# Performance work log

Hardware: AMD Instinct MI355X
Metric: run time of the kernel (lower is better)

The kernel has to match this reference:

```python
import jax, jax.numpy as jnp
import numpy as np

N = 50000      # nodes in the graph (len(vertices))
E = 800000     # edges per adjacency
D = 128        # n_feature (pretrained embedding dim)
V = 100000     # n_input (entity vocab)
OUT = 20       # n_output
L = 7          # n_hidden layers
BN_EPS = 1e-5


def setup_inputs() -> dict:
    key = jax.random.key(0)
    ks = jax.random.split(key, 12)
    s = 1.0 / np.sqrt(D)
    return {
        "vertices": jax.random.randint(ks[0], (N,), 0, V),
        "edge_index": jax.random.randint(ks[1], (L, 2, E), 0, N),
        "edge_weight": jax.random.uniform(ks[2], (L, E), jnp.float32),
        "emb_table": jax.random.normal(ks[3], (V, D), jnp.float32) * 0.02,
        "gcn_w_hidden": jax.random.normal(ks[4], (L - 1, D, D), jnp.float32) * s,
        "gcn_b_hidden": jnp.zeros((L - 1, D), jnp.float32),
        "gcn_w_out": jax.random.normal(ks[5], (D, OUT), jnp.float32) * s,
        "gcn_b_out": jnp.zeros((OUT,), jnp.float32),
        "bn_gamma_hidden": jnp.ones((L - 1, D), jnp.float32),
        "bn_beta_hidden": jnp.zeros((L - 1, D), jnp.float32),
        "bn_gamma_out": jnp.ones((OUT,), jnp.float32),
        "bn_beta_out": jnp.zeros((OUT,), jnp.float32),
        "te_wl": jax.random.normal(ks[6], (L - 1, D, D), jnp.float32) * s,
        "te_wc": jax.random.normal(ks[7], (L - 1, D, D), jnp.float32) * s,
        "te_b": jnp.zeros((L - 1, D), jnp.float32),
        "mask_w": jax.random.normal(ks[8], (V,), jnp.float32) * 0.02,
        "mask_b": jnp.zeros((OUT,), jnp.float32),
    }


def _spmm(src, dst, w, x):
    # out[i] = sum_{e: dst[e]==i} w[e] * x[src[e]]  (sparse adj @ x)
    return jax.ops.segment_sum(w[:, None] * x[src], dst, num_segments=N)


def _batchnorm(x, gamma, beta):
    # BatchNorm1d over the node (batch) axis, training-mode batch statistics
    m = x.mean(axis=0)
    v = x.var(axis=0)
    return (x - m) * jax.lax.rsqrt(v + BN_EPS) * gamma + beta


def reference(vertices, edge_index, edge_weight, emb_table,
              gcn_w_hidden, gcn_b_hidden, gcn_w_out, gcn_b_out,
              bn_gamma_hidden, bn_beta_hidden, bn_gamma_out, bn_beta_out,
              te_wl, te_wc, te_b, mask_w, mask_b):
    x = emb_table[vertices]                               # [N, D]
    for i in range(L):
        last_x = x
        if i < L - 1:
            support = x @ gcn_w_hidden[i]                 # [N, D]
            h = _spmm(edge_index[i, 0], edge_index[i, 1], edge_weight[i], support)
            h = h + gcn_b_hidden[i]
            h = _batchnorm(h, bn_gamma_hidden[i], bn_beta_hidden[i])
            h = jax.nn.relu(h)                            # dropout: eval mode (identity)
            j = (i - 1) % (L - 1)  # faithful to temporal_cells[i-1] (i=0 hits index -1)
            g = jax.nn.sigmoid(last_x @ te_wl[j] + h @ te_wc[j] + te_b[j])
            x = g * h + (1.0 - g) * last_x                # temporal gating cell
        else:
            support = x @ gcn_w_out                       # [N, OUT]
            h = _spmm(edge_index[i, 0], edge_index[i, 1], edge_weight[i], support)
            h = h + gcn_b_out
            x = _batchnorm(h, bn_gamma_out, bn_beta_out)
    x = jax.nn.relu(x)                                    # [N, OUT]
    out = jax.nn.sigmoid(mask_w[vertices] @ x + mask_b)   # MaskLinear + sigmoid -> [OUT]
    return out
```

## Files before the change

kernel.cpp:

```cpp
#include <hip/hip_runtime.h>
#include <hip/hip_fp16.h>

#define NN 50000
#define EE 800000
#define DIM 128
#define OUTC 20
#define LL 7
#define LE (LL*EE)
#define LN (LL*NN)
#define BN_EPS 1e-5f
#define LSTRIDE 136
#define NREP 64
#define NBUK 196
#define GMS  200
#define NBLK 200
#define CH   4000
#define CH4  (CH/4)
#define SCN  (LL*NBUK*NBLK)
#define FSCAP 4864
#define STATSZ (6*NREP*256 + 8*64 + 8*32)
#define STATSZ4 (STATSZ/4)

typedef __attribute__((ext_vector_type(8))) short short8;
typedef __attribute__((ext_vector_type(4))) float f32x4;

static __device__ __forceinline__ float sigm(float z){ return 1.0f/(1.0f+expf(-z)); }
static __device__ __forceinline__ unsigned short f2bf(float f){
  unsigned int u = __float_as_uint(f);
  u += 0x7FFF + ((u>>16)&1);
  return (unsigned short)(u>>16);
}
static __device__ __forceinline__ float bf2f(unsigned short s){
  return __uint_as_float(((unsigned int)s)<<16);
}

__global__ __launch_bounds__(256) void k_pre(const float* __restrict__ wh,
    const float* __restrict__ tewl, const float* __restrict__ tewc,
    const float* __restrict__ wout,
    unsigned short* __restrict__ Wt, unsigned short* __restrict__ WtO,
    const int* __restrict__ ei, int* __restrict__ Gm, float* __restrict__ stats){
  int bid = blockIdx.x;
  int t = threadIdx.x;
  if (bid < 1152){
    int gid = bid*256+t;
    int m = gid>>14; int idx = gid&16383;
    int n = idx>>7, k = idx&127;
    const float* src = (m<6)? wh + (size_t)m*16384
                     : (m<12)? tewl + (size_t)(m-6)*16384
                     : tewc + (size_t)(m-12)*16384;
    Wt[gid] = f2bf(src[k*128+n]);
  } else if (bid < 1168){
    int idx = (bid-1152)*256+t;
    int n = idx>>7, k = idx&127;
    WtO[idx] = (n<OUTC)? f2bf(wout[k*OUTC+n]) : (unsigned short)0;
  } else if (bid < 2568){
    int bb = bid-1168;
    int l = bb / NBLK, b = bb - l*NBLK;
    __shared__ int h[NBUK];
    if (t<NBUK) h[t]=0;
    const int4* dsts = (const int4*)(ei + (size_t)(2*l+1)*EE + b*CH);
    int4 dv[4];
    #pragma unroll
    for (int i=0;i<4;i++){
      int k4 = t + i*256;
      if (k4<CH4) dv[i] = dsts[k4];
    }
    __syncthreads();
    #pragma unroll
    for (int i=0;i<4;i++){
      int k4 = t + i*256;
      if (k4<CH4){
        atomicAdd(&h[dv[i].x>>8], 1);
        atomicAdd(&h[dv[i].y>>8], 1);
        atomicAdd(&h[dv[i].z>>8], 1);
        atomicAdd(&h[dv[i].w>>8], 1);
      }
    }
    __syncthreads();
    int* g = Gm + (size_t)(l*NBLK+b)*GMS;
    if (t<NBUK) g[t]=h[t];
  } else {
    int z = (bid-2568)*256+t;
    if (z < STATSZ4) ((float4*)stats)[z] = make_float4(0.f,0.f,0.f,0.f);
  }
}

__global__ __launch_bounds__(256) void k_scan1p(const int* __restrict__ Gm,
    int* __restrict__ part, int* __restrict__ bsums){
  __shared__ int s[256];
  int t = threadIdx.x;
  int base = blockIdx.x*4096 + t*16;
  int v[16]; int sum = 0;
  #pragma unroll
  for (int i=0;i<16;i++){
    int idx = base+i; int val = 0;
    if (idx < SCN){
      int l = idx/(NBUK*NBLK);
      int r = idx - l*(NBUK*NBLK);
      int buk = r/NBLK, b = r - buk*NBLK;
      val = Gm[(size_t)(l*NBLK+b)*GMS + buk];
    }
    v[i]=val; sum+=val;
  }
  s[t]=sum; __syncthreads();
  for (int off=1; off<256; off<<=1){
    int x = (t>=off)? s[t-off] : 0;
    __syncthreads(); s[t]+=x; __syncthreads();
  }
  if (t==255) bsums[blockIdx.x] = s[255];
  int run = s[t]-sum;
  #pragma unroll
  for (int i=0;i<16;i++){ if (base+i<SCN) part[base+i]=run; run += v[i]; }
}

__global__ __launch_bounds__(1024) void k_scan2(int* bsums, int nb){
  __shared__ int s[1024];
  int t=threadIdx.x;
  int v = (t<nb)? bsums[t]:0;
  s[t]=v; __syncthreads();
  for (int off=1; off<1024; off<<=1){
    int x=(t>=off)? s[t-off]:0; __syncthreads(); s[t]+=x; __syncthreads();
  }
  if (t<nb) bsums[t] = s[t]-v;
}

__global__ __launch_bounds__(256) void k_bscatter(const int* __restrict__ ei,
    const float* __restrict__ ew, const int* __restrict__ S,
    const int* __restrict__ bsums, const int* __restrict__ Gm,
    unsigned int* __restrict__ btmpP, unsigned char* __restrict__ btmpD){
  int l = blockIdx.x / NBLK, b = blockIdx.x - l*NBLK;
  int t = threadIdx.x;
  __shared__ int bstart[NBUK], cur[NBUK], runb[NBUK];
  __shared__ int ps[256];
  __shared__ unsigned int  ebP[CH];
  __shared__ unsigned short ebM[CH];
  const int4*   srcs = (const int4*)(ei + (size_t)(2*l)*EE + b*CH);
  const int4*   dsts = (const int4*)(ei + (size_t)(2*l+1)*EE + b*CH);
  const float4* wsrc = (const float4*)(ew + (size_t)l*EE + b*CH);
  int4 sv[4], dv[4]; float4 wv[4];
  #pragma unroll
  for (int i=0;i<4;i++){
    int k4 = t + i*256;
    if (k4<CH4){
      sv[i] = srcs[k4];
      dv[i] = dsts[k4];
      wv[i] = wsrc[k4];
    }
  }
  int v = (t<NBUK)? Gm[(size_t)(l*NBLK+b)*GMS + t] : 0;
  ps[t]=v; __syncthreads();
  for (int o=1;o<256;o<<=1){ int x=(t>=o)?ps[t-o]:0; __syncthreads(); ps[t]+=x; __syncthreads(); }
  if (t<NBUK){
    bstart[t]=ps[t]-v; cur[t]=ps[t]-v;
    int sidx = (l*NBUK+t)*NBLK + b;
    runb[t] = S[sidx] + bsums[sidx>>12];
  }
  __syncthreads();
  #define PUTE(SRC,DST,WF) { int buk=(DST)>>8; int pos=atomicAdd(&cur[buk],1); \
    unsigned short hw=__half_as_ushort(__float2half(WF)); \
    ebP[pos]=(unsigned)(SRC)|((unsigned)hw<<16); \
    ebM[pos]=(unsigned short)(((DST)&255)|(buk<<8)); }
  #pragma unroll
  for (int i=0;i<4;i++){
    int k4 = t + i*256;
    if (k4<CH4){
      PUTE(sv[i].x, dv[i].x, wv[i].x);
      PUTE(sv[i].y, dv[i].y, wv[i].y);
      PUTE(sv[i].z, dv[i].z, wv[i].z);
      PUTE(sv[i].w, dv[i].w, wv[i].w);
    }
  }
  #undef PUTE
  __syncthreads();
  for (int k=t;k<CH;k+=256){
    unsigned short m = ebM[k];
    int buk = m>>8;
    int gp = runb[buk] + (k - bstart[buk]);
    btmpP[gp] = ebP[k];
    btmpD[gp] = (unsigned char)(m&255);
  }
}

__global__ __launch_bounds__(256) void k_fsort(const unsigned int* __restrict__ btmpP,
    const unsigned char* __restrict__ btmpD, const int* __restrict__ S,
    const int* __restrict__ bsums,
    unsigned int* __restrict__ sedge, int* __restrict__ offs){
  int lbuk = blockIdx.x;
  int l = lbuk/NBUK, bl = lbuk - l*NBUK;
  int t = threadIdx.x;
  int i0 = lbuk*NBLK, i1 = i0+NBLK;
  int base = S[i0] + bsums[i0>>12];
  int end  = (i1==SCN)? LE : (S[i1] + bsums[i1>>12]);
  int nE = end - base;
  __shared__ int cnt[256], sc[256];
  __shared__ unsigned int stg[FSCAP];
  cnt[t]=0;
  __syncthreads();
  for (int k=t; k<nE; k+=256) atomicAdd(&cnt[btmpD[base+k]], 1);
  __syncthreads();
  int c = cnt[t];
  sc[t]=c;
  __syncthreads();
  for (int o=1;o<256;o<<=1){
    int v = (t>=o)? sc[t-o]:0;
    __syncthreads();
    sc[t]+=v;
    __syncthreads();
  }
  int excl = sc[t]-c;
  {
    int node = bl*256+t;
    if (node<NN) offs[(size_t)l*NN+node] = base + excl;
  }
  if (lbuk==0 && t==255) offs[LN]=LE;
  if (nE <= FSCAP){
    cnt[t] = excl;
    __syncthreads();
    for (int k=t; k<nE; k+=256){
      int d = btmpD[base+k];
      int r = atomicAdd(&cnt[d],1);
      stg[r] = btmpP[base+k];
    }
    __syncthreads();
    for (int k=t; k<nE; k+=256) sedge[base+k] = stg[k];
  } else {
    cnt[t] = base + excl;
    __syncthreads();
    for (int k=t; k<nE; k+=256){
      int d = btmpD[base+k];
      int r = atomicAdd(&cnt[d],1);
      sedge[r] = btmpP[base+k];
    }
  }
}

__global__ __launch_bounds__(256) void k_gemm_sup_emb(const int* __restrict__ verts,
    const float* __restrict__ emb, const unsigned short* __restrict__ Wt,
    unsigned short* __restrict__ Y, unsigned short* __restrict__ xout, int M){
  __shared__ unsigned short Xs[32*LSTRIDE];
  int tid = threadIdx.x;
  int row0 = blockIdx.x*32;
  #pragma unroll
  for (int it=0; it<2; it++){
    int idx = tid + it*256;
    int r = idx>>4, k8 = idx&15;
    short8 w = short8(0);
    if (row0+r < M){
      int v = verts[row0+r];
      const float4* p = (const float4*)emb + (size_t)v*32 + k8*2;
      float4 v0 = p[0], v1 = p[1];
      w[0]=(short)f2bf(v0.x); w[1]=(short)f2bf(v0.y); w[2]=(short)f2bf(v0.z); w[3]=(short)f2bf(v0.w);
      w[4]=(short)f2bf(v1.x); w[5]=(short)f2bf(v1.y); w[6]=(short)f2bf(v1.z); w[7]=(short)f2bf(v1.w);
      *(short8*)(xout + (size_t)(row0+r)*128 + k8*8) = w;
    }
    *(short8*)&Xs[r*LSTRIDE + k8*8] = w;
  }
  __syncthreads();
  int w = tid>>6, lane = tid&63, m = lane&15, q = lane>>4;
  int rw = (w&1)*16, cw = (w>>1)*64;
  f32x4 acc[4];
  #pragma unroll
  for (int nt=0;nt<4;nt++){ acc[nt][0]=0.f; acc[nt][1]=0.f; acc[nt][2]=0.f; acc[nt][3]=0.f; }
  #pragma unroll
  for (int kc=0; kc<4; kc++){
    short8 a = *(const short8*)&Xs[(rw+m)*LSTRIDE + kc*32 + 8*q];
    #pragma unroll
    for (int nt=0; nt<4; nt++){
      short8 b = *(const short8*)&Wt[(size_t)(cw+nt*16+m)*128 + kc*32 + 8*q];
      acc[nt] = __builtin_amdgcn_mfma_f32_16x16x32_bf16(a, b, acc[nt], 0,0,0);
    }
  }
  #pragma unroll
  for (int nt=0; nt<4; nt++){
    #pragma unroll
    for (int i=0;i<4;i++){
      int rr = row0 + rw + 4*q + i;
      if (rr<M) Y[(size_t)rr*128 + cw + nt*16 + m] = f2bf(acc[nt][i]);
    }
  }
}

template<int FUSE>
__global__ __launch_bounds__(256,4) void k_gemm_gate2(const unsigned short* __restrict__ H,
    const float* __restrict__ stL,
    const float* __restrict__ gamma, const float* __restrict__ beta,
    const unsigned short* __restrict__ Wl, const unsigned short* __restrict__ Wc,
    const unsigned short* __restrict__ Wn, const float* __restrict__ teb,
    unsigned short* __restrict__ x, unsigned short* __restrict__ supY, int M){
  __shared__ unsigned short XsX[64*LSTRIDE];
  __shared__ unsigned short XsH[64*LSTRIDE];
  __shared__ float sSt[256];
  int tid = threadIdx.x;
  int row0 = blockIdx.x*64;
  int k8 = tid&15;
  float4 g0 = *(const float4*)(gamma + k8*8), g1 = *(const float4*)(gamma + k8*8 + 4);
  float4 b0 = *(const float4*)(beta  + k8*8), b1 = *(const float4*)(beta  + k8*8 + 4);
  short8 xv[4], hv[4];
  #pragma unroll
  for (int it=0; it<4; it++){
    int r = (tid + it*256)>>4;
    xv[it] = short8(0); hv[it] = short8(0);
    if (row0+r < M){
      xv[it] = *(const short8*)(x + (size_t)(row0+r)*128 + k8*8);
      hv[it] = *(const short8*)(H + (size_t)(row0+r)*128 + k8*8);
    }
  }
  {
    float sacc = 0.f;
    #pragma unroll 8
    for (int g=0; g<NREP; g++) sacc += stL[g*256 + tid];
    sSt[tid] = sacc;
  }
  #pragma unroll
  for (int it=0; it<4; it++){
    int r = (tid + it*256)>>4;
    *(short8*)&XsX[r*LSTRIDE + k8*8] = xv[it];
  }
  __syncthreads();
  float scv[8], ofv[8];
  {
    const float gam[8] = {g0.x,g0.y,g0.z,g0.w,g1.x,g1.y,g1.z,g1.w};
    const float bet[8] = {b0.x,b0.y,b0.z,b0.w,b1.x,b1.y,b1.z,b1.w};
    #pragma unroll
    for (int j=0;j<8;j++){
      float s  = sSt[k8*8+j];
      float sq = sSt[128 + k8*8+j];
      float mean = s*(1.0f/NN);
      float var  = sq*(1.0f/NN) - mean*mean;
      float r = rsqrtf(var+BN_EPS)*gam[j];
      scv[j]=r; ofv[j]=bet[j]-mean*r;
    }
  }
  #pragma unroll
  for (int it=0; it<4; it++){
    int r = (tid + it*256)>>4;
    short8 w;
    #pragma unroll
    for (int j=0;j<8;j++){
      float o = bf2f((unsigned short)hv[it][j]);
      w[j] = (short)f2bf(fmaxf(fmaf(o, scv[j], ofv[j]), 0.f));
    }
    *(short8*)&XsH[r*LSTRIDE + k8*8] = w;
  }
  __syncthreads();
  int w = tid>>6, lane = tid&63, m = lane&15, q = lane>>4;
  int rw = (w>>1)*16, cw = (w&1)*64;
  f32x4 acc[2][4];
  #pragma unroll
  for (int rt=0;rt<2;rt++)
    #pragma unroll
    for (int nt=0;nt<4;nt++){ acc[rt][nt][0]=0.f; acc[rt][nt][1]=0.f; acc[rt][nt][2]=0.f; acc[rt][nt][3]=0.f; }
  #pragma unroll
  for (int kc=0; kc<4; kc++){
    short8 a0 = *(const short8*)&XsX[(rw+m)*LSTRIDE + kc*32 + 8*q];
    short8 a1 = *(const short8*)&XsX[(rw+32+m)*LSTRIDE + kc*32 + 8*q];
    #pragma unroll
    for (int nt=0; nt<4; nt++){
      short8 b = *(const short8*)&Wl[(size_t)(cw+nt*16+m)*128 + kc*32 + 8*q];
      acc[0][nt] = __builtin_amdgcn_mfma_f32_16x16x32_bf16(a0, b, acc[0][nt], 0,0,0);
      acc[1][nt] = __builtin_amdgcn_mfma_f32_16x16x32_bf16(a1, b, acc[1][nt], 0,0,0);
    }
  }
  #pragma unroll
  for (int kc=0; kc<4; kc++){
    short8 a0 = *(const short8*)&XsH[(rw+m)*LSTRIDE + kc*32 + 8*q];
    short8 a1 = *(const short8*)&XsH[(rw+32+m)*LSTRIDE + kc*32 + 8*q];
    #pragma unroll
    for (int nt=0; nt<4; nt++){
      short8 b = *(const short8*)&Wc[(size_t)(cw+nt*16+m)*128 + kc*32 + 8*q];
      acc[0][nt] = __builtin_amdgcn_mfma_f32_16x16x32_bf16(a0, b, acc[0][nt], 0,0,0);
      acc[1][nt] = __builtin_amdgcn_mfma_f32_16x16x32_bf16(a1, b, acc[1][nt], 0,0,0);
    }
  }
  __syncthreads();
  #pragma unroll
  for (int rt=0; rt<2; rt++){
    #pragma unroll
    for (int nt=0; nt<4; nt++){
      int col = cw + nt*16 + m;
      float bias = teb[col];
      #pragma unroll
      for (int i=0;i<4;i++){
        int lr = rw + rt*32 + 4*q + i;
        float hvv = bf2f(XsH[lr*LSTRIDE + col]);
        float xo  = bf2f(XsX[lr*LSTRIDE + col]);
        float g = sigm(acc[rt][nt][i] + bias);
        unsigned short xnb = f2bf(g*hvv + (1.f-g)*xo);
        XsH[lr*LSTRIDE + col] = xnb;
        if (FUSE==1) XsX[lr*LSTRIDE + col] = xnb;
      }
    }
  }
  __syncthreads();
  #pragma unroll
  for (int it=0; it<4; it++){
    int r = (tid + it*256)>>4;
    if (row0+r < M)
      *(short8*)(x + (size_t)(row0+r)*128 + k8*8) = *(short8*)&XsH[r*LSTRIDE + k8*8];
  }
  if (FUSE==1){
    #pragma unroll
    for (int rt=0;rt<2;rt++)
      #pragma unroll
      for (int nt=0;nt<4;nt++){ acc[rt][nt][0]=0.f; acc[rt][nt][1]=0.f; acc[rt][nt][2]=0.f; acc[rt][nt][3]=0.f; }
    #pragma unroll
    for (int kc=0; kc<4; kc++){
      short8 a0 = *(const short8*)&XsX[(rw+m)*LSTRIDE + kc*32 + 8*q];
      short8 a1 = *(const short8*)&XsX[(rw+32+m)*LSTRIDE + kc*32 + 8*q];
      #pragma unroll
      for (int nt=0; nt<4; nt++){
        short8 b = *(const short8*)&Wn[(size_t)(cw+nt*16+m)*128 + kc*32 + 8*q];
        acc[0][nt] = __builtin_amdgcn_mfma_f32_16x16x32_bf16(a0, b, acc[0][nt], 0,0,0);
        acc[1][nt] = __builtin_amdgcn_mfma_f32_16x16x32_bf16(a1, b, acc[1][nt], 0,0,0);
      }
    }
    #pragma unroll
    for (int rt=0; rt<2; rt++){
      #pragma unroll
      for (int nt=0; nt<4; nt++){
        #pragma unroll
        for (int i=0;i<4;i++){
          int rr = row0 + rw + rt*32 + 4*q + i;
          if (rr<M) supY[(size_t)rr*128 + cw + nt*16 + m] = f2bf(acc[rt][nt][i]);
        }
      }
    }
  }
  if (FUSE==2){
    if (cw==0){
      f32x4 ao0[2], ao1[2];
      #pragma unroll
      for (int nt=0;nt<2;nt++){
        ao0[nt][0]=0.f; ao0[nt][1]=0.f; ao0[nt][2]=0.f; ao0[nt][3]=0.f;
        ao1[nt][0]=0.f; ao1[nt][1]=0.f; ao1[nt][2]=0.f; ao1[nt][3]=0.f;
      }
      #pragma unroll
      for (int kc=0; kc<4; kc++){
        short8 a0 = *(const short8*)&XsH[(rw+m)*LSTRIDE + kc*32 + 8*q];
        short8 a1 = *(const short8*)&XsH[(rw+32+m)*LSTRIDE + kc*32 + 8*q];
        #pragma unroll
        for (int nt=0; nt<2; nt++){
          short8 b = *(const short8*)&Wn[(size_t)(nt*16+m)*128 + kc*32 + 8*q];
          ao0[nt] = __builtin_amdgcn_mfma_f32_16x16x32_bf16(a0, b, ao0[nt], 0,0,0);
          ao1[nt] = __builtin_amdgcn_mfma_f32_16x16x32_bf16(a1, b, ao1[nt], 0,0,0);
        }
      }
      #pragma unroll
      for (int rt=0; rt<2; rt++){
        #pragma unroll
        for (int nt=0; nt<2; nt++){
          #pragma unroll
          for (int i=0;i<4;i++){
            int rr = row0 + rw + rt*32 + 4*q + i;
            float v = rt? ao1[nt][i] : ao0[nt][i];
            if (rr<M) supY[(size_t)rr*32 + nt*16 + m] = f2bf(v);
          }
        }
      }
    }
  }
}

__global__ __launch_bounds__(256) void k_spmm128(const unsigned short* __restrict__ sup,
    const unsigned int* __restrict__ sedge, const int* __restrict__ offs,
    unsigned short* __restrict__ h, int lbase, float* __restrict__ stL){
  int nl = threadIdx.x>>5;
  int node = blockIdx.x*8 + nl;
  int fq = threadIdx.x & 31;
  int p = offs[lbase+node], end = offs[lbase+node+1];
  float4 a0 = make_float4(0.f,0.f,0.f,0.f), a1 = a0, a2 = a0, a3 = a0;
  for (; p+7<end; p+=8){
    unsigned int ev[8];
    #pragma unroll
    for (int u=0;u<8;u++) ev[u] = __builtin_nontemporal_load(sedge+p+u);
    ushort4 sv[8];
    #pragma unroll
    for (int u=0;u<8;u++) sv[u] = *(const ushort4*)(sup + (size_t)(ev[u]&0xFFFFu)*128 + fq*4);
    #pragma unroll
    for (int u=0;u<8;u++){
      float w = __half2float(__ushort_as_half((unsigned short)(ev[u]>>16)));
      float4& a = (u&3)==0? a0 : (u&3)==1? a1 : (u&3)==2? a2 : a3;
      a.x += w*bf2f(sv[u].x); a.y += w*bf2f(sv[u].y);
      a.z += w*bf2f(sv[u].z); a.w += w*bf2f(sv[u].w);
    }
  }
  for (; p+3<end; p+=4){
    unsigned int e0 = __builtin_nontemporal_load(sedge+p);
    unsigned int e1 = __builtin_nontemporal_load(sedge+p+1);
    unsigned int e2 = __builtin_nontemporal_load(sedge+p+2);
    unsigned int e3 = __builtin_nontemporal_load(sedge+p+3);
    ushort4 s0 = *(const ushort4*)(sup + (size_t)(e0&0xFFFFu)*128 + fq*4);
    ushort4 s1 = *(const ushort4*)(sup + (size_t)(e1&0xFFFFu)*128 + fq*4);
    ushort4 s2 = *(const ushort4*)(sup + (size_t)(e2&0xFFFFu)*128 + fq*4);
    ushort4 s3 = *(const ushort4*)(sup + (size_t)(e3&0xFFFFu)*128 + fq*4);
    float w0 = __half2float(__ushort_as_half((unsigned short)(e0>>16)));
    float w1 = __half2float(__ushort_as_half((unsigned short)(e1>>16)));
    float w2 = __half2float(__ushort_as_half((unsigned short)(e2>>16)));
    float w3 = __half2float(__ushort_as_half((unsigned short)(e3>>16)));
    a0.x += w0*bf2f(s0.x); a0.y += w0*bf2f(s0.y); a0.z += w0*bf2f(s0.z); a0.w += w0*bf2f(s0.w);
    a1.x += w1*bf2f(s1.x); a1.y += w1*bf2f(s1.y); a1.z += w1*bf2f(s1.z); a1.w += w1*bf2f(s1.w);
    a2.x += w2*bf2f(s2.x); a2.y += w2*bf2f(s2.y); a2.z += w2*bf2f(s2.z); a2.w += w2*bf2f(s2.w);
    a3.x += w3*bf2f(s3.x); a3.y += w3*bf2f(s3.y); a3.z += w3*bf2f(s3.z); a3.w += w3*bf2f(s3.w);
  }
  for (; p<end; p++){
    unsigned int e0 = __builtin_nontemporal_load(sedge+p);
    float w0 = __half2float(__ushort_as_half((unsigned short)(e0>>16)));
    ushort4 s0 = *(const ushort4*)(sup + (size_t)(e0&0xFFFFu)*128 + fq*4);
    a0.x += w0*bf2f(s0.x); a0.y += w0*bf2f(s0.y); a0.z += w0*bf2f(s0.z); a0.w += w0*bf2f(s0.w);
  }
  a0.x+=a1.x+a2.x+a3.x; a0.y+=a1.y+a2.y+a3.y;
  a0.z+=a1.z+a2.z+a3.z; a0.w+=a1.w+a2.w+a3.w;
  ushort4 ov;
  ov.x=f2bf(a0.x); ov.y=f2bf(a0.y); ov.z=f2bf(a0.z); ov.w=f2bf(a0.w);
  *(ushort4*)(h + (size_t)node*128 + fq*4) = ov;
  __shared__ float sP[8][132], sQ[8][132];
  int f0 = fq*4;
  sP[nl][f0+0]=a0.x; sP[nl][f0+1]=a0.y; sP[nl][f0+2]=a0.z; sP[nl][f0+3]=a0.w;
  sQ[nl][f0+0]=a0.x*a0.x; sQ[nl][f0+1]=a0.y*a0.y; sQ[nl][f0+2]=a0.z*a0.z; sQ[nl][f0+3]=a0.w*a0.w;
  __syncthreads();
  if (threadIdx.x < 128){
    int f = threadIdx.x;
    float s=0.f, sq=0.f;
    #pragma unroll
    for (int n=0;n<8;n++){ s += sP[n][f]; sq += sQ[n][f]; }
    float* base = stL + (blockIdx.x & (NREP-1))*256;
    atomicAdd(&base[f], s); atomicAdd(&base[128+f], sq);
  }
}

__global__ __launch_bounds__(256) void k_spmm_out(const unsigned short* __restrict__ sup,
    const unsigned int* __restrict__ sedge, const int* __restrict__ offs,
    float* __restrict__ h, int lbase, float* __restrict__ st8){
  int nl = threadIdx.x>>5;
  int node = blockIdx.x*8 + nl;
  int c = threadIdx.x & 31;
  bool act = c < OUTC;
  int p = offs[lbase+node], end = offs[lbase+node+1];
  float a0=0.f,a1=0.f,a2=0.f,a3=0.f;
  for (; p+7<end; p+=8){
    unsigned int ev[8];
    #pragma unroll
    for (int u=0;u<8;u++) ev[u] = __builtin_nontemporal_load(sedge+p+u);
    float sv[8];
    #pragma unroll
    for (int u=0;u<8;u++) sv[u] = bf2f(sup[(size_t)(ev[u]&0xFFFFu)*32 + c]);
    #pragma unroll
    for (int u=0;u<8;u++){
      float w = __half2float(__ushort_as_half((unsigned short)(ev[u]>>16)));
      if ((u&3)==0) a0 += w*sv[u];
      else if ((u&3)==1) a1 += w*sv[u];
      else if ((u&3)==2) a2 += w*sv[u];
      else a3 += w*sv[u];
    }
  }
  for (; p<end; p++){
    unsigned int e = __builtin_nontemporal_load(sedge+p);
    float w = __half2float(__ushort_as_half((unsigned short)(e>>16)));
    a0 += w*bf2f(sup[(size_t)(e&0xFFFFu)*32 + c]);
  }
  float v = a0+a1+a2+a3;
  if (act) h[(size_t)node*OUTC+c] = v;
  if (!act) v = 0.f;
  __shared__ float sS[8][33], sQ[8][33];
  sS[nl][c] = v; sQ[nl][c] = v*v;
  __syncthreads();
  if (threadIdx.x < 32){
    float s=0.f, sq=0.f;
    #pragma unroll
    for (int n=0;n<8;n++){ s += sS[n][c]; sq += sQ[n][c]; }
    if (c<OUTC){
      float* base = st8 + (blockIdx.x&7)*64;
      atomicAdd(&base[c], s); atomicAdd(&base[32+c], sq);
    }
  }
}

__global__ __launch_bounds__(256) void k_reduce(const float* __restrict__ xf,
    const float* __restrict__ st8, const float* __restrict__ gamma,
    const float* __restrict__ beta, const int* __restrict__ verts,
    const float* __restrict__ mw, float* __restrict__ acc8, int rpb){
  int c = threadIdx.x & 31, g = threadIdx.x >> 5;
  float scn=0.f, offc=0.f;
  if (c<OUTC){
    float s=0.f, sq=0.f;
    #pragma unroll
    for (int i=0;i<8;i++){ s += st8[i*64+c]; sq += st8[i*64+32+c]; }
    const float invN = 1.0f/NN;
    float m = s*invN;
    float var = sq*invN - m*m;
    scn = rsqrtf(var+BN_EPS)*gamma[c];
    offc = beta[c] - m*scn;
  }
  int r0 = blockIdx.x*rpb;
  int r1 = min(NN, r0+rpb);
  float s=0.f;
  for (int r=r0+g; r<r1; r+=8){
    float m = mw[verts[r]];
    if (c<OUTC){
      float v = fmaxf(fmaf(xf[(size_t)r*OUTC+c], scn, offc), 0.f);
      s += m * v;
    }
  }
  __shared__ float sh[256];
  sh[threadIdx.x]=s; __syncthreads();
  if (threadIdx.x<32){
    #pragma unroll
    for (int i=1;i<8;i++) s += sh[threadIdx.x + i*32];
    if (c<OUTC) atomicAdd(&acc8[(blockIdx.x&7)*32 + c], s);
  }
}

__global__ void k_final(const float* __restrict__ acc8, const float* __restrict__ mb,
                        float* __restrict__ out){
  int c=threadIdx.x;
  if (c<OUTC){
    float s=0.f;
    #pragma unroll
    for (int g=0; g<8; g++) s += acc8[g*32+c];
    out[c] = sigm(s+mb[c]);
  }
}

extern "C" void kernel_launch(void* const* d_in, const int* in_sizes, int n_in,
                              void* d_out, int out_size, void* d_ws, size_t ws_size,
                              hipStream_t stream){
  const int*   verts = (const int*)d_in[0];
  const int*   ei    = (const int*)d_in[1];
  const float* ew    = (const float*)d_in[2];
  const float* emb   = (const float*)d_in[3];
  const float* wh    = (const float*)d_in[4];
  const float* w_out = (const float*)d_in[6];
  const float* bng_h = (const float*)d_in[8];
  const float* bnb_h = (const float*)d_in[9];
  const float* bng_o = (const float*)d_in[10];
  const float* bnb_o = (const float*)d_in[11];
  const float* tewl  = (const float*)d_in[12];
  const float* tewc  = (const float*)d_in[13];
  const float* teb   = (const float*)d_in[14];
  const float* maskw = (const float*)d_in[15];
  const float* maskb = (const float*)d_in[16];
  float* out = (float*)d_out;

  char* ws = (char*)d_ws;
  size_t off=0;
  auto alloc=[&](size_t bytes)->char*{ char* p = ws+off; off += (bytes+255)&~(size_t)255; return p; };
  unsigned int* sedge = (unsigned int*)alloc(sizeof(int)*LE);
  int*   offs   = (int*)  alloc(sizeof(int)*(LN+1));
  int*   Gm     = (int*)  alloc(sizeof(int)*LL*NBLK*GMS);
  int*   S      = (int*)  alloc(sizeof(int)*(SCN+1));
  int*   bsums  = (int*)  alloc(sizeof(int)*1024);
  unsigned short* xbf   = (unsigned short*)alloc(sizeof(short)*NN*DIM);
  unsigned short* supbf = (unsigned short*)alloc(sizeof(short)*NN*DIM);
  unsigned short* hbf   = (unsigned short*)alloc(sizeof(short)*NN*DIM);
  unsigned short* supO  = (unsigned short*)alloc(sizeof(short)*NN*32);
  unsigned short* Wt = (unsigned short*)alloc(sizeof(short)*18*DIM*DIM);
  unsigned short* WtO = (unsigned short*)alloc(sizeof(short)*32*DIM);
  float* stats  = (float*)alloc(sizeof(float)*STATSZ);
  float* ostat8 = stats + 6*NREP*256;
  float* racc8  = ostat8 + 8*64;
  unsigned int*  btmpP = (unsigned int*)xbf;
  unsigned char* btmpD = (unsigned char*)hbf;

  k_pre<<<2665,256,0,stream>>>(wh, tewl, tewc, w_out, Wt, WtO, ei, Gm, stats);
  int nsb = (SCN+4095)/4096;
  k_scan1p<<<nsb,256,0,stream>>>(Gm, S, bsums);
  k_scan2<<<1,1024,0,stream>>>(bsums, nsb);
  k_bscatter<<<LL*NBLK,256,0,stream>>>(ei, ew, S, bsums, Gm, btmpP, btmpD);
  k_fsort<<<LL*NBUK,256,0,stream>>>(btmpP, btmpD, S, bsums, sedge, offs);

  k_gemm_sup_emb<<<(NN+31)/32,256,0,stream>>>(verts, emb, Wt, supbf, xbf, NN);
  for (int i=0;i<6;i++){
    int j = (i==0)?5:(i-1);
    float* stL = stats + i*NREP*256;
    k_spmm128<<<NN/8,256,0,stream>>>(supbf, sedge, offs, hbf, i*NN, stL);
    if (i<5)
      k_gemm_gate2<1><<<(NN+63)/64,256,0,stream>>>(hbf, stL,
          bng_h+(size_t)i*DIM, bnb_h+(size_t)i*DIM,
          Wt + (size_t)(6+j)*DIM*DIM, Wt + (size_t)(12+j)*DIM*DIM,
          Wt + (size_t)(i+1)*DIM*DIM, teb + (size_t)j*DIM, xbf, supbf, NN);
    else
      k_gemm_gate2<2><<<(NN+63)/64,256,0,stream>>>(hbf, stL,
          bng_h+(size_t)i*DIM, bnb_h+(size_t)i*DIM,
          Wt + (size_t)(6+j)*DIM*DIM, Wt + (size_t)(12+j)*DIM*DIM,
          WtO, teb + (size_t)j*DIM, xbf, supO, NN);
  }

  k_spmm_out<<<NN/8,256,0,stream>>>(supO, sedge, offs, (float*)hbf, 6*NN, ostat8);
  float* bufO = (float*)hbf;
  k_reduce<<<512,256,0,stream>>>(bufO, ostat8, bng_o, bnb_o, verts, maskw, racc8, 98);
  k_final<<<1,64,0,stream>>>(racc8, maskb, out);
}
```

Before: 702.5 us.

## Use wave-shuffle scans, retile gate GEMM per wave, fuse final sigmoid into reduce

Replaces the shared-memory Hillis-Steele prefix scans in the bucket scatter and fine sort kernels with wave-level shuffle scans plus a small cross-wave fixup, removing most barriers. Retiles the gate GEMM so each of the four waves owns a 32-column strip over all 64 rows, loading B fragments once per k-chunk and reusing them across four row tiles. The final sigmoid kernel is folded into k_reduce with a last-block ticket counter, saving one launch. The ticket relies on the stats buffer being zeroed each call, which is assumed to happen in k_pre.

```diff
diff --git a/kernel.cpp b/kernel.cpp
--- a/kernel.cpp
+++ b/kernel.cpp
@@ -18,7 +18,7 @@
 #define CH4  (CH/4)
 #define SCN  (LL*NBUK*NBLK)
 #define FSCAP 4864
-#define STATSZ (6*NREP*256 + 8*64 + 8*32)
+#define STATSZ (6*NREP*256 + 8*64 + 8*32 + 8)
 #define STATSZ4 (STATSZ/4)
 
 typedef __attribute__((ext_vector_type(8))) short short8;
@@ -131,7 +131,7 @@
   int l = blockIdx.x / NBLK, b = blockIdx.x - l*NBLK;
   int t = threadIdx.x;
   __shared__ int bstart[NBUK], cur[NBUK], runb[NBUK];
-  __shared__ int ps[256];
+  __shared__ int wsum[4];
   __shared__ unsigned int  ebP[CH];
   __shared__ unsigned short ebM[CH];
   const int4*   srcs = (const int4*)(ei + (size_t)(2*l)*EE + b*CH);
@@ -148,10 +148,23 @@
     }
   }
   int v = (t<NBUK)? Gm[(size_t)(l*NBLK+b)*GMS + t] : 0;
-  ps[t]=v; __syncthreads();
-  for (int o=1;o<256;o<<=1){ int x=(t>=o)?ps[t-o]:0; __syncthreads(); ps[t]+=x; __syncthreads(); }
+  int incl = v;
+  #pragma unroll
+  for (int d=1; d<64; d<<=1){
+    int n = __shfl_up(incl, d, 64);
+    if ((t&63) >= d) incl += n;
+  }
+  if ((t&63)==63) wsum[t>>6] = incl;
+  __syncthreads();
+  {
+    int wv_ = t>>6, add = 0;
+    if (wv_>0) add += wsum[0];
+    if (wv_>1) add += wsum[1];
+    if (wv_>2) add += wsum[2];
+    incl += add;
+  }
   if (t<NBUK){
-    bstart[t]=ps[t]-v; cur[t]=ps[t]-v;
+    bstart[t]=incl-v; cur[t]=incl-v;
     int sidx = (l*NBUK+t)*NBLK + b;
     runb[t] = S[sidx] + bsums[sidx>>12];
   }
@@ -192,22 +205,30 @@
   int base = S[i0] + bsums[i0>>12];
   int end  = (i1==SCN)? LE : (S[i1] + bsums[i1>>12]);
   int nE = end - base;
-  __shared__ int cnt[256], sc[256];
+  __shared__ int cnt[256];
+  __shared__ int wsum[4];
   __shared__ unsigned int stg[FSCAP];
   cnt[t]=0;
   __syncthreads();
   for (int k=t; k<nE; k+=256) atomicAdd(&cnt[btmpD[base+k]], 1);
   __syncthreads();
   int c = cnt[t];
-  sc[t]=c;
-  __syncthreads();
-  for (int o=1;o<256;o<<=1){
-    int v = (t>=o)? sc[t-o]:0;
-    __syncthreads();
-    sc[t]+=v;
-    __syncthreads();
-  }
-  int excl = sc[t]-c;
+  int incl = c;
+  #pragma unroll
+  for (int d=1; d<64; d<<=1){
+    int n = __shfl_up(incl, d, 64);
+    if ((t&63) >= d) incl += n;
+  }
+  if ((t&63)==63) wsum[t>>6] = incl;
+  __syncthreads();
+  {
+    int wv_ = t>>6, add = 0;
+    if (wv_>0) add += wsum[0];
+    if (wv_>1) add += wsum[1];
+    if (wv_>2) add += wsum[2];
+    incl += add;
+  }
+  int excl = incl - c;
   {
     int node = bl*256+t;
     if (node<NN) offs[(size_t)l*NN+node] = base + excl;
@@ -293,8 +314,11 @@
   int tid = threadIdx.x;
   int row0 = blockIdx.x*64;
   int k8 = tid&15;
+  int w = tid>>6, lane = tid&63, m = lane&15, q = lane>>4;
+  int cw = w*32;
   float4 g0 = *(const float4*)(gamma + k8*8), g1 = *(const float4*)(gamma + k8*8 + 4);
-  float4 b0 = *(const float4*)(beta  + k8*8), b1 = *(const float4*)(beta  + k8*8 + 4);
+  float4 b0v = *(const float4*)(beta  + k8*8), b1v = *(const float4*)(beta  + k8*8 + 4);
+  float tb0 = teb[cw+m], tb1 = teb[cw+16+m];
   short8 xv[4], hv[4];
   #pragma unroll
   for (int it=0; it<4; it++){
@@ -320,7 +344,7 @@
   float scv[8], ofv[8];
   {
     const float gam[8] = {g0.x,g0.y,g0.z,g0.w,g1.x,g1.y,g1.z,g1.w};
-    const float bet[8] = {b0.x,b0.y,b0.z,b0.w,b1.x,b1.y,b1.z,b1.w};
+    const float bet[8] = {b0v.x,b0v.y,b0v.z,b0v.w,b1v.x,b1v.y,b1v.z,b1v.w};
     #pragma unroll
     for (int j=0;j<8;j++){
       float s  = sSt[k8*8+j];
@@ -334,54 +358,52 @@
   #pragma unroll
   for (int it=0; it<4; it++){
     int r = (tid + it*256)>>4;
-    short8 w;
+    short8 wv_;
     #pragma unroll
     for (int j=0;j<8;j++){
       float o = bf2f((unsigned short)hv[it][j]);
-      w[j] = (short)f2bf(fmaxf(fmaf(o, scv[j], ofv[j]), 0.f));
-    }
-    *(short8*)&XsH[r*LSTRIDE + k8*8] = w;
-  }
-  __syncthreads();
-  int w = tid>>6, lane = tid&63, m = lane&15, q = lane>>4;
-  int rw = (w>>1)*16, cw = (w&1)*64;
-  f32x4 acc[2][4];
-  #pragma unroll
-  for (int rt=0;rt<2;rt++)
-    #pragma unroll
-    for (int nt=0;nt<4;nt++){ acc[rt][nt][0]=0.f; acc[rt][nt][1]=0.f; acc[rt][nt][2]=0.f; acc[rt][nt][3]=0.f; }
+      wv_[j] = (short)f2bf(fmaxf(fmaf(o, scv[j], ofv[j]), 0.f));
+    }
+    *(short8*)&XsH[r*LSTRIDE + k8*8] = wv_;
+  }
+  __syncthreads();
+  f32x4 acc[4][2];
+  #pragma unroll
+  for (int rt=0;rt<4;rt++)
+    #pragma unroll
+    for (int nt=0;nt<2;nt++){ acc[rt][nt][0]=0.f; acc[rt][nt][1]=0.f; acc[rt][nt][2]=0.f; acc[rt][nt][3]=0.f; }
   #pragma unroll
   for (int kc=0; kc<4; kc++){
-    short8 a0 = *(const short8*)&XsX[(rw+m)*LSTRIDE + kc*32 + 8*q];
-    short8 a1 = *(const short8*)&XsX[(rw+32+m)*LSTRIDE + kc*32 + 8*q];
-    #pragma unroll
-    for (int nt=0; nt<4; nt++){
-      short8 b = *(const short8*)&Wl[(size_t)(cw+nt*16+m)*128 + kc*32 + 8*q];
-      acc[0][nt] = __builtin_amdgcn_mfma_f32_16x16x32_bf16(a0, b, acc[0][nt], 0,0,0);
-      acc[1][nt] = __builtin_amdgcn_mfma_f32_16x16x32_bf16(a1, b, acc[1][nt], 0,0,0);
+    short8 b0 = *(const short8*)&Wl[(size_t)(cw+m)*128 + kc*32 + 8*q];
+    short8 b1 = *(const short8*)&Wl[(size_t)(cw+16+m)*128 + kc*32 + 8*q];
+    #pragma unroll
+    for (int rt=0; rt<4; rt++){
+      short8 a = *(const short8*)&XsX[(rt*16+m)*LSTRIDE + kc*32 + 8*q];
+      acc[rt][0] = __builtin_amdgcn_mfma_f32_16x16x32_bf16(a, b0, acc[rt][0], 0,0,0);
+      acc[rt][1] = __builtin_amdgcn_mfma_f32_16x16x32_bf16(a, b1, acc[rt][1], 0,0,0);
     }
   }
   #pragma unroll
   for (int kc=0; kc<4; kc++){
-    short8 a0 = *(const short8*)&XsH[(rw+m)*LSTRIDE + kc*32 + 8*q];
-    short8 a1 = *(const short8*)&XsH[(rw+32+m)*LSTRIDE + kc*32 + 8*q];
-    #pragma unroll
-    for (int nt=0; nt<4; nt++){
-      short8 b = *(const short8*)&Wc[(size_t)(cw+nt*16+m)*128 + kc*32 + 8*q];
-      acc[0][nt] = __builtin_amdgcn_mfma_f32_16x16x32_bf16(a0, b, acc[0][nt], 0,0,0);
-      acc[1][nt] = __builtin_amdgcn_mfma_f32_16x16x32_bf16(a1, b, acc[1][nt], 0,0,0);
-    }
-  }
-  __syncthreads();
-  #pragma unroll
-  for (int rt=0; rt<2; rt++){
-    #pragma unroll
-    for (int nt=0; nt<4; nt++){
+    short8 b0 = *(const short8*)&Wc[(size_t)(cw+m)*128 + kc*32 + 8*q];
+    short8 b1 = *(const short8*)&Wc[(size_t)(cw+16+m)*128 + kc*32 + 8*q];
+    #pragma unroll
+    for (int rt=0; rt<4; rt++){
+      short8 a = *(const short8*)&XsH[(rt*16+m)*LSTRIDE + kc*32 + 8*q];
+      acc[rt][0] = __builtin_amdgcn_mfma_f32_16x16x32_bf16(a, b0, acc[rt][0], 0,0,0);
+      acc[rt][1] = __builtin_amdgcn_mfma_f32_16x16x32_bf16(a, b1, acc[rt][1], 0,0,0);
+    }
+  }
+  __syncthreads();
+  #pragma unroll
+  for (int rt=0; rt<4; rt++){
+    #pragma unroll
+    for (int nt=0; nt<2; nt++){
       int col = cw + nt*16 + m;
-      float bias = teb[col];
+      float bias = nt? tb1 : tb0;
       #pragma unroll
       for (int i=0;i<4;i++){
-        int lr = rw + rt*32 + 4*q + i;
+        int lr = rt*16 + 4*q + i;
         float hvv = bf2f(XsH[lr*LSTRIDE + col]);
         float xo  = bf2f(XsX[lr*LSTRIDE + col]);
         float g = sigm(acc[rt][nt][i] + bias);
@@ -400,49 +422,48 @@
   }
   if (FUSE==1){
     #pragma unroll
-    for (int rt=0;rt<2;rt++)
+    for (int rt=0;rt<4;rt++)
       #pragma unroll
-      for (int nt=0;nt<4;nt++){ acc[rt][nt][0]=0.f; acc[rt][nt][1]=0.f; acc[rt][nt][2]=0.f; acc[rt][nt][3]=0.f; }
+      for (int nt=0;nt<2;nt++){ acc[rt][nt][0]=0.f; acc[rt][nt][1]=0.f; acc[rt][nt][2]=0.f; acc[rt][nt][3]=0.f; }
     #pragma unroll
     for (int kc=0; kc<4; kc++){
-      short8 a0 = *(const short8*)&XsX[(rw+m)*LSTRIDE + kc*32 + 8*q];
-      short8 a1 = *(const short8*)&XsX[(rw+32+m)*LSTRIDE + kc*32 + 8*q];
+      short8 b0 = *(const short8*)&Wn[(size_t)(cw+m)*128 + kc*32 + 8*q];
+      short8 b1 = *(const short8*)&Wn[(size_t)(cw+16+m)*128 + kc*32 + 8*q];
       #pragma unroll
-      for (int nt=0; nt<4; nt++){
-        short8 b = *(const short8*)&Wn[(size_t)(cw+nt*16+m)*128 + kc*32 + 8*q];
-        acc[0][nt] = __builtin_amdgcn_mfma_f32_16x16x32_bf16(a0, b, acc[0][nt], 0,0,0);
-        acc[1][nt] = __builtin_amdgcn_mfma_f32_16x16x32_bf16(a1, b, acc[1][nt], 0,0,0);
+      for (int rt=0; rt<4; rt++){
+        short8 a = *(const short8*)&XsX[(rt*16+m)*LSTRIDE + kc*32 + 8*q];
+        acc[rt][0] = __builtin_amdgcn_mfma_f32_16x16x32_bf16(a, b0, acc[rt][0], 0,0,0);
+        acc[rt][1] = __builtin_amdgcn_mfma_f32_16x16x32_bf16(a, b1, acc[rt][1], 0,0,0);
       }
     }
     #pragma unroll
-    for (int rt=0; rt<2; rt++){
+    for (int rt=0; rt<4; rt++){
       #pragma unroll
-      for (int nt=0; nt<4; nt++){
+      for (int nt=0; nt<2; nt++){
         #pragma unroll
         for (int i=0;i<4;i++){
-          int rr = row0 + rw + rt*32 + 4*q + i;
+          int rr = row0 + rt*16 + 4*q + i;
           if (rr<M) supY[(size_t)rr*128 + cw + nt*16 + m] = f2bf(acc[rt][nt][i]);
         }
       }
     }
   }
   if (FUSE==2){
-    if (cw==0){
-      f32x4 ao0[2], ao1[2];
+    if (w < 2){
+      f32x4 ao[2][2];
       #pragma unroll
-      for (int nt=0;nt<2;nt++){
-        ao0[nt][0]=0.f; ao0[nt][1]=0.f; ao0[nt][2]=0.f; ao0[nt][3]=0.f;
-        ao1[nt][0]=0.f; ao1[nt][1]=0.f; ao1[nt][2]=0.f; ao1[nt][3]=0.f;
-      }
+      for (int rt=0;rt<2;rt++)
+        #pragma unroll
+        for (int nt=0;nt<2;nt++){ ao[rt][nt][0]=0.f; ao[rt][nt][1]=0.f; ao[rt][nt][2]=0.f; ao[rt][nt][3]=0.f; }
       #pragma unroll
       for (int kc=0; kc<4; kc++){
-        short8 a0 = *(const short8*)&XsH[(rw+m)*LSTRIDE + kc*32 + 8*q];
-        short8 a1 = *(const short8*)&XsH[(rw+32+m)*LSTRIDE + kc*32 + 8*q];
+        short8 b0 = *(const short8*)&Wn[(size_t)(m)*128 + kc*32 + 8*q];
+        short8 b1 = *(const short8*)&Wn[(size_t)(16+m)*128 + kc*32 + 8*q];
         #pragma unroll
-        for (int nt=0; nt<2; nt++){
-          short8 b = *(const short8*)&Wn[(size_t)(nt*16+m)*128 + kc*32 + 8*q];
-          ao0[nt] = __builtin_amdgcn_mfma_f32_16x16x32_bf16(a0, b, ao0[nt], 0,0,0);
-          ao1[nt] = __builtin_amdgcn_mfma_f32_16x16x32_bf16(a1, b, ao1[nt], 0,0,0);
+        for (int rt=0; rt<2; rt++){
+          short8 a = *(const short8*)&XsH[((w*2+rt)*16+m)*LSTRIDE + kc*32 + 8*q];
+          ao[rt][0] = __builtin_amdgcn_mfma_f32_16x16x32_bf16(a, b0, ao[rt][0], 0,0,0);
+          ao[rt][1] = __builtin_amdgcn_mfma_f32_16x16x32_bf16(a, b1, ao[rt][1], 0,0,0);
         }
       }
       #pragma unroll
@@ -451,9 +472,8 @@
         for (int nt=0; nt<2; nt++){
           #pragma unroll
           for (int i=0;i<4;i++){
-            int rr = row0 + rw + rt*32 + 4*q + i;
-            float v = rt? ao1[nt][i] : ao0[nt][i];
-            if (rr<M) supY[(size_t)rr*32 + nt*16 + m] = f2bf(v);
+            int rr = row0 + (w*2+rt)*16 + 4*q + i;
+            if (rr<M) supY[(size_t)rr*32 + nt*16 + m] = f2bf(ao[rt][nt][i]);
           }
         }
       }
@@ -578,7 +598,9 @@
 __global__ __launch_bounds__(256) void k_reduce(const float* __restrict__ xf,
     const float* __restrict__ st8, const float* __restrict__ gamma,
     const float* __restrict__ beta, const int* __restrict__ verts,
-    const float* __restrict__ mw, float* __restrict__ acc8, int rpb){
+    const float* __restrict__ mw, float* __restrict__ acc8, int rpb,
+    const float* __restrict__ mb, float* __restrict__ outp, int* __restrict__ tick,
+    int nblocks){
   int c = threadIdx.x & 31, g = threadIdx.x >> 5;
   float scn=0.f, offc=0.f;
   if (c<OUTC){
@@ -608,16 +630,20 @@
     for (int i=1;i<8;i++) s += sh[threadIdx.x + i*32];
     if (c<OUTC) atomicAdd(&acc8[(blockIdx.x&7)*32 + c], s);
   }
-}
-
-__global__ void k_final(const float* __restrict__ acc8, const float* __restrict__ mb,
-                        float* __restrict__ out){
-  int c=threadIdx.x;
-  if (c<OUTC){
-    float s=0.f;
-    #pragma unroll
-    for (int g=0; g<8; g++) s += acc8[g*32+c];
-    out[c] = sigm(s+mb[c]);
+  __syncthreads();
+  __shared__ int lastf;
+  if (threadIdx.x==0){
+    __threadfence();
+    int tk = __hip_atomic_fetch_add(tick, 1, __ATOMIC_ACQ_REL, __HIP_MEMORY_SCOPE_AGENT);
+    lastf = (tk == nblocks-1);
+  }
+  __syncthreads();
+  if (lastf && threadIdx.x < 32 && c < OUTC){
+    float s2=0.f;
+    #pragma unroll
+    for (int gg=0; gg<8; gg++)
+      s2 += __hip_atomic_load(&acc8[gg*32+c], __ATOMIC_RELAXED, __HIP_MEMORY_SCOPE_AGENT);
+    outp[c] = sigm(s2+mb[c]);
   }
 }
 
@@ -658,6 +684,7 @@
   float* stats  = (float*)alloc(sizeof(float)*STATSZ);
   float* ostat8 = stats + 6*NREP*256;
   float* racc8  = ostat8 + 8*64;
+  int*   tick   = (int*)(racc8 + 8*32);
   unsigned int*  btmpP = (unsigned int*)xbf;
   unsigned char* btmpD = (unsigned char*)hbf;
 
@@ -687,6 +714,6 @@
 
   k_spmm_out<<<NN/8,256,0,stream>>>(supO, sedge, offs, (float*)hbf, 6*NN, ostat8);
   float* bufO = (float*)hbf;
-  k_reduce<<<512,256,0,stream>>>(bufO, ostat8, bng_o, bnb_o, verts, maskw, racc8, 98);
-  k_final<<<1,64,0,stream>>>(racc8, maskb, out);
-}
+  k_reduce<<<512,256,0,stream>>>(bufO, ostat8, bng_o, bnb_o, verts, maskw, racc8, 98,
+                                 maskb, out, tick, 512);
+}
```

After: 655.5 us. 1.07x faster.
